# Kernel optimization log

Measured on AMD Instinct MI355X. Metric: run time of the kernel, lower is better.

## Reference

```python
import jax, jax.numpy as jnp
import numpy as np

EMBED_DIM = 1024
HEADS = 16
HEAD_DIM = EMBED_DIM // HEADS


def setup_inputs() -> dict:
    key = jax.random.key(0)
    ks = jax.random.split(key, 9)
    B, T, C = 4, 4096, EMBED_DIM
    s = 1.0 / np.sqrt(C)
    inp = {
        "x": jax.random.normal(ks[0], (B, T, C), dtype=jnp.float32),
        "Wq": jax.random.normal(ks[1], (C, C), dtype=jnp.float32) * s,
        "bq": jnp.zeros((C,), dtype=jnp.float32),
        "Wk": jax.random.normal(ks[2], (C, C), dtype=jnp.float32) * s,
        "bk": jnp.zeros((C,), dtype=jnp.float32),
        "Wv": jax.random.normal(ks[3], (C, C), dtype=jnp.float32) * s,
        "bv": jnp.zeros((C,), dtype=jnp.float32),
        "Wc": jax.random.normal(ks[4], (C, C), dtype=jnp.float32) * s,
        "bc": jnp.zeros((C,), dtype=jnp.float32),
    }
    return inp


def reference(x, Wq, bq, Wk, bk, Wv, bv, Wc, bc):
    B, T, C = x.shape
    H, D = HEADS, HEAD_DIM
    # projections (torch Linear: x @ W.T + b)
    q = (x @ Wq.T + bq).reshape(B, T, H, D).transpose(0, 2, 1, 3)  # [B,H,T,D]
    k = (x @ Wk.T + bk).reshape(B, T, H, D).transpose(0, 2, 1, 3)
    v = (x @ Wv.T + bv).reshape(B, T, H, D).transpose(0, 2, 1, 3)
    # ELU+1 feature map
    q = jax.nn.elu(q) + 1.0
    k = jax.nn.elu(k) + 1.0
    # kv outer product: [B,H,D,D]
    kv = jnp.einsum("bhtd,bhte->bhde", k, v)
    # normalizer: q @ sum_t k  -> [B,H,T,1]
    k_sum = k.sum(axis=2)  # [B,H,D]
    z = 1.0 / (jnp.einsum("bhtd,bhd->bht", q, k_sum)[..., None] + 1e-6)
    y = jnp.einsum("bhtd,bhde->bhte", q, kv) * z  # [B,H,T,D]
    y = y.transpose(0, 2, 1, 3).reshape(B, T, C)
    return y @ Wc.T + bc
```

## Files before the change

kernel.cpp:

```cpp
#include <hip/hip_runtime.h>
#include <math.h>

#define EMBED 1024
#define HEADS 16
#define HD 64
#define BATCH 4
#define TSEQ 4096
#define BH (BATCH * HEADS)
#define MROWS (BATCH * TSEQ)

typedef _Float16 f16;
typedef __attribute__((ext_vector_type(4))) _Float16 f16x4;
typedef __attribute__((ext_vector_type(8))) _Float16 f16x8;
typedef __attribute__((ext_vector_type(4))) float f32x4;

#define GLOBAL_AS __attribute__((address_space(1)))
#define LDS_AS __attribute__((address_space(3)))

__device__ __forceinline__ float elu1(float v) {
    return v > 0.f ? v + 1.f : __expf(v);
}

__device__ __forceinline__ int swzc(int row, int col, int cols) {
    int g = (col >> 3) ^ (row & 7);
    return row * cols + (g << 3) + (col & 7);
}

__device__ __forceinline__ f16x8 fragld(const f16* t, int row, int k, int cols) {
    return *(const f16x8*)&t[swzc(row, k, cols)];
}

__device__ __forceinline__ f32x4 mfma16(f16x8 a, f16x8 b, f32x4 c) {
    return __builtin_amdgcn_mfma_f32_16x16x32_f16(a, b, c, 0, 0, 0);
}

__device__ __forceinline__ void gld_lds16(const f16* g, f16* l) {
    __builtin_amdgcn_global_load_lds((const GLOBAL_AS void*)g, (LDS_AS void*)l, 16, 0, 0);
}

__global__ __launch_bounds__(256) void prep(
    const float* __restrict__ x, f16* __restrict__ xh,
    const float* __restrict__ Wq, const float* __restrict__ Wk,
    const float* __restrict__ Wv, const float* __restrict__ Wc,
    const float* __restrict__ bq, const float* __restrict__ bk,
    const float* __restrict__ bv, const float* __restrict__ bc,
    f16* __restrict__ Wall, float* __restrict__ ball, float* __restrict__ kvz)
{
    int bid = blockIdx.x;
    if (bid < 16384) {
        size_t i4 = (size_t)bid * 256 + threadIdx.x;
        float4 f = *(const float4*)&x[i4 * 4];
        f16x4 h = {(f16)f.x, (f16)f.y, (f16)f.z, (f16)f.w};
        *(f16x4*)&xh[i4 * 4] = h;
    } else {
        int i4 = (bid - 16384) * 256 + threadIdx.x;
        int cls = i4 >> 18;
        const float* W = cls == 0 ? Wq : cls == 1 ? Wk : cls == 2 ? Wv : Wc;
        int off = (i4 & 0x3FFFF) * 4;
        float4 f = *(const float4*)&W[off];
        f16x4 h = {(f16)f.x, (f16)f.y, (f16)f.z, (f16)f.w};
        *(f16x4*)&Wall[(size_t)i4 * 4] = h;
        if (i4 < 4096) {
            int c2 = i4 >> 10;
            const float* bb = c2 == 0 ? bq : c2 == 1 ? bk : c2 == 2 ? bv : bc;
            ball[i4] = bb[i4 & 1023];
        }
        if (i4 < 66560) {
            *(float4*)&kvz[i4 * 4] = (float4){0.f, 0.f, 0.f, 0.f};
        }
    }
}

__global__ __launch_bounds__(256) void gemm_qkv(
    const f16* __restrict__ xh, const f16* __restrict__ Wall,
    const float* __restrict__ ball,
    f16* __restrict__ q, f16* __restrict__ kT, f16* __restrict__ vT)
{
    __shared__ __align__(16) f16 As[128 * 64];
    __shared__ __align__(16) f16 Bs[128 * 64];

    const int tid = threadIdx.x, lane = tid & 63, w = tid >> 6;
    const int wr = w >> 1, wc4 = w & 1, l15 = lane & 15, l4 = lane >> 4;

    const int orig = blockIdx.x;
    const int xcd = orig & 7;
    const int local = orig >> 3;
    const int ntile = local >> 4;
    const int mloc = local & 15;
    const int m0 = (xcd * 16 + mloc) * 128;
    const int n0 = ntile * 128;
    const int cls = n0 >> 10;

    const int gcol = ((lane & 7) ^ (lane >> 3)) << 3;
    const int rsub = lane >> 3;
    const size_t arow = (size_t)(m0 + w * 32 + rsub) * EMBED + gcol;
    const size_t brow = (size_t)(n0 + w * 32 + rsub) * EMBED + gcol;

    f32x4 acc[4][4];
    #pragma unroll
    for (int i = 0; i < 4; ++i)
        #pragma unroll
        for (int j = 0; j < 4; ++j) acc[i][j] = (f32x4){0.f, 0.f, 0.f, 0.f};

    for (int k0 = 0; k0 < EMBED; k0 += 64) {
        #pragma unroll
        for (int c = 0; c < 4; ++c) {
            gld_lds16(&xh[arow + (size_t)c * 8 * EMBED + k0], &As[(w * 4 + c) * 512]);
            gld_lds16(&Wall[brow + (size_t)c * 8 * EMBED + k0], &Bs[(w * 4 + c) * 512]);
        }
        __syncthreads();
        #pragma unroll
        for (int kk = 0; kk < 64; kk += 32) {
            f16x8 af[4], bf[4];
            #pragma unroll
            for (int i = 0; i < 4; ++i)
                af[i] = fragld(As, wr * 64 + i * 16 + l15, kk + l4 * 8, 64);
            #pragma unroll
            for (int j = 0; j < 4; ++j)
                bf[j] = fragld(Bs, wc4 * 64 + j * 16 + l15, kk + l4 * 8, 64);
            #pragma unroll
            for (int i = 0; i < 4; ++i)
                #pragma unroll
                for (int j = 0; j < 4; ++j)
                    acc[i][j] = mfma16(af[i], bf[j], acc[i][j]);
        }
        __syncthreads();
    }

    if (cls == 0) {
        #pragma unroll
        for (int j = 0; j < 4; ++j) {
            int c = n0 + wc4 * 64 + j * 16 + l15;
            float bj = ball[c];
            #pragma unroll
            for (int i = 0; i < 4; ++i) {
                #pragma unroll
                for (int r = 0; r < 4; ++r) {
                    int t = m0 + wr * 64 + i * 16 + l4 * 4 + r;
                    q[(size_t)t * EMBED + c] = (f16)elu1(acc[i][j][r] + bj);
                }
            }
        }
    } else {
        f16* dst = (cls == 1) ? kT : vT;
        const bool act = (cls == 1);
        #pragma unroll
        for (int j = 0; j < 4; ++j) {
            int n = n0 + wc4 * 64 + j * 16 + l15;
            int d = n & 1023;
            float bj = ball[n];
            #pragma unroll
            for (int i = 0; i < 4; ++i) {
                int t = m0 + wr * 64 + i * 16 + l4 * 4;
                f16x4 hv;
                #pragma unroll
                for (int r = 0; r < 4; ++r) {
                    float v = acc[i][j][r] + bj;
                    if (act) v = elu1(v);
                    hv[r] = (f16)v;
                }
                *(f16x4*)&dst[(size_t)d * MROWS + t] = hv;
            }
        }
    }
}

__global__ __launch_bounds__(256) void kv_ksum(
    const f16* __restrict__ kT, const f16* __restrict__ vT,
    float* __restrict__ kvg, float* __restrict__ ksg)
{
    __shared__ __align__(16) f16 kl[64 * 128];
    __shared__ __align__(16) f16 vl[64 * 128];

    const int bh = blockIdx.x, b = bh >> 4, h = bh & 15;
    const int tid = threadIdx.x, lane = tid & 63, w = tid >> 6;
    const int l15 = lane & 15, l4 = lane >> 4;
    const int tbase = b * TSEQ + blockIdx.y * 512;

    f32x4 kvacc[4];
    #pragma unroll
    for (int j = 0; j < 4; ++j) kvacc[j] = (f32x4){0.f, 0.f, 0.f, 0.f};
    float ksacc = 0.f;

    for (int ss = 0; ss < 4; ++ss) {
        const int tg = tbase + ss * 128;
        #pragma unroll
        for (int c = 0; c < 4; ++c) {
            int idx = tid + c * 256;
            int row = idx >> 4, t8 = (idx & 15) << 3;
            f16x8 a = *(const f16x8*)&kT[(size_t)(h * 64 + row) * MROWS + tg + t8];
            *(f16x8*)&kl[swzc(row, t8, 128)] = a;
            f16x8 bb = *(const f16x8*)&vT[(size_t)(h * 64 + row) * MROWS + tg + t8];
            *(f16x8*)&vl[swzc(row, t8, 128)] = bb;
        }
        __syncthreads();
        #pragma unroll
        for (int kk = 0; kk < 128; kk += 32) {
            f16x8 a = fragld(vl, 16 * w + l15, kk + l4 * 8, 128);
            #pragma unroll
            for (int j = 0; j < 4; ++j) {
                f16x8 bfr = fragld(kl, j * 16 + l15, kk + l4 * 8, 128);
                kvacc[j] = mfma16(a, bfr, kvacc[j]);
            }
        }
        {
            int d = tid & 63, qq = tid >> 6;
            #pragma unroll
            for (int t8 = 0; t8 < 32; t8 += 8) {
                f16x8 kv8 = fragld(kl, d, qq * 32 + t8, 128);
                #pragma unroll
                for (int e = 0; e < 8; ++e) ksacc += (float)kv8[e];
            }
        }
        __syncthreads();
    }

    #pragma unroll
    for (int j = 0; j < 4; ++j)
        #pragma unroll
        for (int r = 0; r < 4; ++r)
            atomicAdd(&kvg[(size_t)bh * 4096 +
                           (size_t)(16 * w + l4 * 4 + r) * HD + j * 16 + l15],
                      kvacc[j][r]);
    atomicAdd(&ksg[bh * HD + (tid & 63)], ksacc);
}

__global__ __launch_bounds__(256) void y_kernel(
    const f16* __restrict__ q, const float* __restrict__ kvg,
    const float* __restrict__ ksg, f16* __restrict__ y)
{
    __shared__ __align__(16) f16 qs[128 * 64];
    __shared__ __align__(16) f16 kvs[64 * 64];
    __shared__ __align__(16) f16 ylds[128 * 64];
    __shared__ float kss[64];
    __shared__ float zs[128];

    const int bh = blockIdx.x, b = bh >> 4, h = bh & 15;
    const int tid = threadIdx.x, lane = tid & 63, w = tid >> 6;
    const int l15 = lane & 15, l4 = lane >> 4;
    const int t0g = b * TSEQ + blockIdx.y * 128;

    #pragma unroll
    for (int c = 0; c < 4; ++c) {
        int idx = tid + c * 256;
        int row = idx >> 3, col8 = (idx & 7) << 3;
        f16x8 v = *(const f16x8*)&q[(size_t)(t0g + row) * EMBED + h * 64 + col8];
        *(f16x8*)&qs[swzc(row, col8, 64)] = v;
    }
    #pragma unroll
    for (int c = 0; c < 4; ++c) {
        int idx = tid + c * 256;
        int e = idx >> 4, d4 = (idx & 15) << 2;
        float4 f = *(const float4*)&kvg[(size_t)bh * 4096 + e * 64 + d4];
        f16x4 hv = {(f16)f.x, (f16)f.y, (f16)f.z, (f16)f.w};
        *(f16x4*)&kvs[swzc(e, d4, 64)] = hv;
    }
    if (tid < 64) kss[tid] = ksg[bh * HD + tid];
    __syncthreads();

    {
        int t = tid >> 1, dh = (tid & 1) * 32;
        float s = 0.f;
        #pragma unroll
        for (int d8 = 0; d8 < 32; d8 += 8) {
            f16x8 qv = fragld(qs, t, dh + d8, 64);
            #pragma unroll
            for (int e = 0; e < 8; ++e) s += (float)qv[e] * kss[dh + d8 + e];
        }
        s += __shfl_xor(s, 1);
        if ((tid & 1) == 0) zs[t] = 1.f / (s + 1e-6f);
    }
    __syncthreads();

    f32x4 yacc[8];
    #pragma unroll
    for (int jn = 0; jn < 8; ++jn) yacc[jn] = (f32x4){0.f, 0.f, 0.f, 0.f};
    #pragma unroll
    for (int kk = 0; kk < 64; kk += 32) {
        f16x8 a = fragld(kvs, 16 * w + l15, kk + l4 * 8, 64);
        #pragma unroll
        for (int jn = 0; jn < 8; ++jn) {
            f16x8 bq8 = fragld(qs, jn * 16 + l15, kk + l4 * 8, 64);
            yacc[jn] = mfma16(a, bq8, yacc[jn]);
        }
    }
    #pragma unroll
    for (int jn = 0; jn < 8; ++jn) {
        int t = jn * 16 + l15;
        float z = zs[t];
        int e0 = 16 * w + l4 * 4;
        f16x4 hv;
        #pragma unroll
        for (int r = 0; r < 4; ++r) hv[r] = (f16)(yacc[jn][r] * z);
        *(f16x4*)&ylds[swzc(t, e0, 64)] = hv;
    }
    __syncthreads();

    {
        int row = tid >> 1, eh = (tid & 1) * 32;
        size_t gb = (size_t)(t0g + row) * EMBED + h * 64 + eh;
        #pragma unroll
        for (int c8 = 0; c8 < 32; c8 += 8) {
            f16x8 v = fragld(ylds, row, eh + c8, 64);
            *(f16x8*)&y[gb + c8] = v;
        }
    }
}

__global__ __launch_bounds__(256) void gemm_out(
    const f16* __restrict__ y, const f16* __restrict__ Wall,
    const float* __restrict__ ball, float* __restrict__ out)
{
    __shared__ __align__(16) f16 As[128 * 64];
    __shared__ __align__(16) f16 Bs[128 * 64];

    const int tid = threadIdx.x, lane = tid & 63, w = tid >> 6;
    const int wr = w >> 1, wc4 = w & 1, l15 = lane & 15, l4 = lane >> 4;

    const int orig = blockIdx.x;
    const int xcd = orig & 7;
    const int local = orig >> 3;
    const int ntile = local >> 4;
    const int mloc = local & 15;
    const int m0 = (xcd * 16 + mloc) * 128;
    const int n0 = ntile * 128;

    const int gcol = ((lane & 7) ^ (lane >> 3)) << 3;
    const int rsub = lane >> 3;
    const size_t arow = (size_t)(m0 + w * 32 + rsub) * EMBED + gcol;
    const size_t brow = (size_t)(3072 + n0 + w * 32 + rsub) * EMBED + gcol;

    f32x4 acc[4][4];
    #pragma unroll
    for (int i = 0; i < 4; ++i)
        #pragma unroll
        for (int j = 0; j < 4; ++j) acc[i][j] = (f32x4){0.f, 0.f, 0.f, 0.f};

    for (int k0 = 0; k0 < EMBED; k0 += 64) {
        #pragma unroll
        for (int c = 0; c < 4; ++c) {
            gld_lds16(&y[arow + (size_t)c * 8 * EMBED + k0], &As[(w * 4 + c) * 512]);
            gld_lds16(&Wall[brow + (size_t)c * 8 * EMBED + k0], &Bs[(w * 4 + c) * 512]);
        }
        __syncthreads();
        #pragma unroll
        for (int kk = 0; kk < 64; kk += 32) {
            f16x8 af[4], bf[4];
            #pragma unroll
            for (int i = 0; i < 4; ++i)
                af[i] = fragld(As, wr * 64 + i * 16 + l15, kk + l4 * 8, 64);
            #pragma unroll
            for (int j = 0; j < 4; ++j)
                bf[j] = fragld(Bs, wc4 * 64 + j * 16 + l15, kk + l4 * 8, 64);
            #pragma unroll
            for (int i = 0; i < 4; ++i)
                #pragma unroll
                for (int j = 0; j < 4; ++j)
                    acc[i][j] = mfma16(af[i], bf[j], acc[i][j]);
        }
        __syncthreads();
    }

    #pragma unroll
    for (int j = 0; j < 4; ++j) {
        int n = n0 + wc4 * 64 + j * 16 + l15;
        float bj = ball[3072 + n];
        #pragma unroll
        for (int i = 0; i < 4; ++i) {
            #pragma unroll
            for (int r = 0; r < 4; ++r) {
                int m = m0 + wr * 64 + i * 16 + l4 * 4 + r;
                out[(size_t)m * EMBED + n] = acc[i][j][r] + bj;
            }
        }
    }
}

extern "C" void kernel_launch(void* const* d_in, const int* in_sizes, int n_in,
                              void* d_out, int out_size, void* d_ws, size_t ws_size,
                              hipStream_t stream) {
    (void)in_sizes; (void)n_in; (void)out_size; (void)ws_size;
    const float* x  = (const float*)d_in[0];
    const float* Wq = (const float*)d_in[1];
    const float* bq = (const float*)d_in[2];
    const float* Wk = (const float*)d_in[3];
    const float* bk = (const float*)d_in[4];
    const float* Wv = (const float*)d_in[5];
    const float* bv = (const float*)d_in[6];
    const float* Wc = (const float*)d_in[7];
    const float* bc = (const float*)d_in[8];
    float* out = (float*)d_out;

    char* W = (char*)d_ws;
    f16* xh   = (f16*)W;
    f16* q_ws = (f16*)(W + 33554432);
    f16* kT   = (f16*)(W + 67108864);
    f16* vT   = (f16*)(W + 100663296);
    f16* Wall = (f16*)(W + 134217728);
    float* ball = (float*)(W + 142606336);
    float* kvg  = (float*)(W + 142622720);
    float* ksg  = (float*)(W + 143671296);

    prep<<<20480, 256, 0, stream>>>(x, xh, Wq, Wk, Wv, Wc, bq, bk, bv, bc,
                                    Wall, ball, kvg);

    gemm_qkv<<<3072, 256, 0, stream>>>(xh, Wall, ball, q_ws, kT, vT);

    kv_ksum<<<dim3(BH, 8), 256, 0, stream>>>(kT, vT, kvg, ksg);

    y_kernel<<<dim3(BH, TSEQ / 128), 256, 0, stream>>>(q_ws, kvg, ksg, q_ws);

    gemm_out<<<1024, 256, 0, stream>>>(q_ws, Wall, ball, out);
}
```

Baseline: 241.1 us.

## Fuse KV outer-product and k-sum into QKV GEMM epilogue, stage Q stores through LDS

The QKV GEMM now tiles N so that each K/V block covers one head's K and V columns together. Its epilogue computes the per-tile k^T v product and k column sums straight from LDS and atomically adds them into kvg/ksg. This removes the kT/vT round trip through global memory and the separate kv_ksum kernel. Q outputs are also staged through swizzled LDS for coalesced 16-byte stores, and the XCD-aware block remapping is replaced with a plain 2D grid, which may hurt L2 locality and adds many more atomics.

Result: faster. 226.2 us (-6.2%).

```diff
diff --git a/kernel.cpp b/kernel.cpp
--- a/kernel.cpp
+++ b/kernel.cpp
@@ -74,27 +74,30 @@
 __global__ __launch_bounds__(256) void gemm_qkv(
     const f16* __restrict__ xh, const f16* __restrict__ Wall,
     const float* __restrict__ ball,
-    f16* __restrict__ q, f16* __restrict__ kT, f16* __restrict__ vT)
+    f16* __restrict__ q, float* __restrict__ kvg, float* __restrict__ ksg)
 {
-    __shared__ __align__(16) f16 As[128 * 64];
-    __shared__ __align__(16) f16 Bs[128 * 64];
+    __shared__ __align__(16) f16 smem[2 * 128 * 64];
+    f16* As = smem;
+    f16* Bs = smem + 128 * 64;
 
     const int tid = threadIdx.x, lane = tid & 63, w = tid >> 6;
     const int wr = w >> 1, wc4 = w & 1, l15 = lane & 15, l4 = lane >> 4;
 
-    const int orig = blockIdx.x;
-    const int xcd = orig & 7;
-    const int local = orig >> 3;
-    const int ntile = local >> 4;
-    const int mloc = local & 15;
-    const int m0 = (xcd * 16 + mloc) * 128;
-    const int n0 = ntile * 128;
-    const int cls = n0 >> 10;
+    const int m0 = blockIdx.x * 128;
+    const int ny = blockIdx.y;
+    const bool isq = (ny < 8);
+    const int h = ny - 8;
 
     const int gcol = ((lane & 7) ^ (lane >> 3)) << 3;
     const int rsub = lane >> 3;
     const size_t arow = (size_t)(m0 + w * 32 + rsub) * EMBED + gcol;
-    const size_t brow = (size_t)(n0 + w * 32 + rsub) * EMBED + gcol;
+
+    const int wrow = w * 32 + rsub;
+    int brow_idx;
+    if (isq)          brow_idx = ny * 128 + wrow;
+    else if (wrow < 64) brow_idx = 1024 + h * 64 + wrow;
+    else                brow_idx = 2048 + h * 64 + (wrow - 64);
+    const size_t brow = (size_t)brow_idx * EMBED + gcol;
 
     f32x4 acc[4][4];
     #pragma unroll
@@ -127,102 +130,85 @@
         __syncthreads();
     }
 
-    if (cls == 0) {
+    if (isq) {
+        const int n0 = ny * 128;
         #pragma unroll
         for (int j = 0; j < 4; ++j) {
-            int c = n0 + wc4 * 64 + j * 16 + l15;
-            float bj = ball[c];
+            int c = wc4 * 64 + j * 16 + l15;
+            float bj = ball[n0 + c];
             #pragma unroll
             for (int i = 0; i < 4; ++i) {
                 #pragma unroll
                 for (int r = 0; r < 4; ++r) {
-                    int t = m0 + wr * 64 + i * 16 + l4 * 4 + r;
-                    q[(size_t)t * EMBED + c] = (f16)elu1(acc[i][j][r] + bj);
+                    int t = wr * 64 + i * 16 + l4 * 4 + r;
+                    smem[swzc(t, c, 128)] = (f16)elu1(acc[i][j][r] + bj);
                 }
             }
         }
+        __syncthreads();
+        #pragma unroll
+        for (int p = 0; p < 8; ++p) {
+            int idx = tid + p * 256;
+            int row = idx >> 4, g8 = (idx & 15) << 3;
+            f16x8 v = *(const f16x8*)&smem[swzc(row, g8, 128)];
+            *(f16x8*)&q[(size_t)(m0 + row) * EMBED + n0 + g8] = v;
+        }
     } else {
-        f16* dst = (cls == 1) ? kT : vT;
-        const bool act = (cls == 1);
+        f16* kt = As;
+        f16* vt = Bs;
+        const float* biasp = ball + (wc4 ? 2048 : 1024) + h * 64;
         #pragma unroll
         for (int j = 0; j < 4; ++j) {
-            int n = n0 + wc4 * 64 + j * 16 + l15;
-            int d = n & 1023;
-            float bj = ball[n];
+            int d = j * 16 + l15;
+            float bj = biasp[d];
+            f16* dst = wc4 ? vt : kt;
             #pragma unroll
             for (int i = 0; i < 4; ++i) {
-                int t = m0 + wr * 64 + i * 16 + l4 * 4;
+                int t0 = wr * 64 + i * 16 + l4 * 4;
                 f16x4 hv;
                 #pragma unroll
                 for (int r = 0; r < 4; ++r) {
-                    float v = acc[i][j][r] + bj;
-                    if (act) v = elu1(v);
-                    hv[r] = (f16)v;
+                    float vv = acc[i][j][r] + bj;
+                    if (!wc4) vv = elu1(vv);
+                    hv[r] = (f16)vv;
                 }
-                *(f16x4*)&dst[(size_t)d * MROWS + t] = hv;
-            }
-        }
-    }
-}
-
-__global__ __launch_bounds__(256) void kv_ksum(
-    const f16* __restrict__ kT, const f16* __restrict__ vT,
-    float* __restrict__ kvg, float* __restrict__ ksg)
-{
-    __shared__ __align__(16) f16 kl[64 * 128];
-    __shared__ __align__(16) f16 vl[64 * 128];
-
-    const int bh = blockIdx.x, b = bh >> 4, h = bh & 15;
-    const int tid = threadIdx.x, lane = tid & 63, w = tid >> 6;
-    const int l15 = lane & 15, l4 = lane >> 4;
-    const int tbase = b * TSEQ + blockIdx.y * 512;
-
-    f32x4 kvacc[4];
-    #pragma unroll
-    for (int j = 0; j < 4; ++j) kvacc[j] = (f32x4){0.f, 0.f, 0.f, 0.f};
-    float ksacc = 0.f;
-
-    for (int ss = 0; ss < 4; ++ss) {
-        const int tg = tbase + ss * 128;
-        #pragma unroll
-        for (int c = 0; c < 4; ++c) {
-            int idx = tid + c * 256;
-            int row = idx >> 4, t8 = (idx & 15) << 3;
-            f16x8 a = *(const f16x8*)&kT[(size_t)(h * 64 + row) * MROWS + tg + t8];
-            *(f16x8*)&kl[swzc(row, t8, 128)] = a;
-            f16x8 bb = *(const f16x8*)&vT[(size_t)(h * 64 + row) * MROWS + tg + t8];
-            *(f16x8*)&vl[swzc(row, t8, 128)] = bb;
-        }
-        __syncthreads();
-        #pragma unroll
-        for (int kk = 0; kk < 128; kk += 32) {
-            f16x8 a = fragld(vl, 16 * w + l15, kk + l4 * 8, 128);
+                *(f16x4*)&dst[swzc(d, t0, 128)] = hv;
+            }
+        }
+        __syncthreads();
+
+        f32x4 kvacc[4];
+        #pragma unroll
+        for (int j = 0; j < 4; ++j) kvacc[j] = (f32x4){0.f, 0.f, 0.f, 0.f};
+        #pragma unroll
+        for (int tc = 0; tc < 4; ++tc) {
+            f16x8 a = fragld(vt, 16 * w + l15, tc * 32 + l4 * 8, 128);
             #pragma unroll
             for (int j = 0; j < 4; ++j) {
-                f16x8 bfr = fragld(kl, j * 16 + l15, kk + l4 * 8, 128);
+                f16x8 bfr = fragld(kt, j * 16 + l15, tc * 32 + l4 * 8, 128);
                 kvacc[j] = mfma16(a, bfr, kvacc[j]);
             }
         }
+        float ksacc = 0.f;
         {
-            int d = tid & 63, qq = tid >> 6;
+            int d = tid & 63, q4 = tid >> 6;
             #pragma unroll
             for (int t8 = 0; t8 < 32; t8 += 8) {
-                f16x8 kv8 = fragld(kl, d, qq * 32 + t8, 128);
-                #pragma unroll
-                for (int e = 0; e < 8; ++e) ksacc += (float)kv8[e];
-            }
-        }
-        __syncthreads();
-    }
-
-    #pragma unroll
-    for (int j = 0; j < 4; ++j)
-        #pragma unroll
-        for (int r = 0; r < 4; ++r)
-            atomicAdd(&kvg[(size_t)bh * 4096 +
-                           (size_t)(16 * w + l4 * 4 + r) * HD + j * 16 + l15],
-                      kvacc[j][r]);
-    atomicAdd(&ksg[bh * HD + (tid & 63)], ksacc);
+                f16x8 k8 = fragld(kt, d, q4 * 32 + t8, 128);
+                #pragma unroll
+                for (int e = 0; e < 8; ++e) ksacc += (float)k8[e];
+            }
+        }
+        const int bh = (m0 >> 12) * HEADS + h;
+        #pragma unroll
+        for (int j = 0; j < 4; ++j)
+            #pragma unroll
+            for (int r = 0; r < 4; ++r)
+                atomicAdd(&kvg[(size_t)bh * 4096 +
+                               (size_t)(16 * w + l4 * 4 + r) * HD + j * 16 + l15],
+                          kvacc[j][r]);
+        atomicAdd(&ksg[bh * HD + (tid & 63)], ksacc);
+    }
 }
 
 __global__ __launch_bounds__(256) void y_kernel(
@@ -316,14 +302,8 @@
 
     const int tid = threadIdx.x, lane = tid & 63, w = tid >> 6;
     const int wr = w >> 1, wc4 = w & 1, l15 = lane & 15, l4 = lane >> 4;
-
-    const int orig = blockIdx.x;
-    const int xcd = orig & 7;
-    const int local = orig >> 3;
-    const int ntile = local >> 4;
-    const int mloc = local & 15;
-    const int m0 = (xcd * 16 + mloc) * 128;
-    const int n0 = ntile * 128;
+    const int m0 = blockIdx.x * 128;
+    const int n0 = blockIdx.y * 128;
 
     const int gcol = ((lane & 7) ^ (lane >> 3)) << 3;
     const int rsub = lane >> 3;
@@ -394,21 +374,17 @@
     char* W = (char*)d_ws;
     f16* xh   = (f16*)W;
     f16* q_ws = (f16*)(W + 33554432);
-    f16* kT   = (f16*)(W + 67108864);
-    f16* vT   = (f16*)(W + 100663296);
-    f16* Wall = (f16*)(W + 134217728);
-    float* ball = (float*)(W + 142606336);
-    float* kvg  = (float*)(W + 142622720);
-    float* ksg  = (float*)(W + 143671296);
+    f16* Wall = (f16*)(W + 67108864);
+    float* ball = (float*)(W + 75497472);
+    float* kvg  = (float*)(W + 75513856);
+    float* ksg  = (float*)(W + 76562432);
 
     prep<<<20480, 256, 0, stream>>>(x, xh, Wq, Wk, Wv, Wc, bq, bk, bv, bc,
                                     Wall, ball, kvg);
 
-    gemm_qkv<<<3072, 256, 0, stream>>>(xh, Wall, ball, q_ws, kT, vT);
-
-    kv_ksum<<<dim3(BH, 8), 256, 0, stream>>>(kT, vT, kvg, ksg);
+    gemm_qkv<<<dim3(128, 24), 256, 0, stream>>>(xh, Wall, ball, q_ws, kvg, ksg);
 
     y_kernel<<<dim3(BH, TSEQ / 128), 256, 0, stream>>>(q_ws, kvg, ksg, q_ws);
 
-    gemm_out<<<1024, 256, 0, stream>>>(q_ws, Wall, ball, out);
-}
+    gemm_out<<<dim3(128, 8), 256, 0, stream>>>(q_ws, Wall, ball, out);
+}
```
